# Performance work log

Hardware: AMD Instinct MI355X
Metric: run time of the kernel (lower is better)

The kernel has to match this reference:

```python
import jax, jax.numpy as jnp
import numpy as np

HIDDEN = 1024
N_EXPERTS = 8
CAP_FACTOR = 1.1
LN_EPS = 1e-5


def setup_inputs() -> dict:
    key = jax.random.key(0)
    ks = jax.random.split(key, 8)
    d, E, dff = HIDDEN, N_EXPERTS, 4 * HIDDEN
    x = jax.random.normal(ks[0], (4, 2048, d), dtype=jnp.float32)
    gate_w = jax.random.normal(ks[1], (d, E), dtype=jnp.float32) / np.sqrt(d)
    ln_g = jnp.ones((E, d), dtype=jnp.float32)
    ln_b = jnp.zeros((E, d), dtype=jnp.float32)
    w1 = jax.random.normal(ks[2], (E, d, dff), dtype=jnp.float32) / np.sqrt(d)
    b1 = jnp.zeros((E, dff), dtype=jnp.float32)
    w2 = jax.random.normal(ks[3], (E, dff, d), dtype=jnp.float32) / np.sqrt(dff)
    b2 = jnp.zeros((E, d), dtype=jnp.float32)
    return {"x": x, "gate_w": gate_w, "ln_g": ln_g, "ln_b": ln_b,
            "w1": w1, "b1": b1, "w2": w2, "b2": b2}


def reference(x, gate_w, ln_g, ln_b, w1, b1, w2, b2):
    B, S, d = x.shape
    E = gate_w.shape[1]
    N = B * S
    cap = int(N / E * CAP_FACTOR)  # expert capacity

    xt = x.reshape(N, d)
    # Router: top-1 expert per token (max-subtract before softmax is a no-op)
    logits = xt @ gate_w                               # [N, E]
    probs = jax.nn.softmax(logits, axis=-1)
    eidx = jnp.argmax(probs, axis=-1)                  # [N] int

    onehot = jax.nn.one_hot(eidx, E, dtype=jnp.int32)  # [N, E]
    counts = onehot.sum(axis=0).astype(jnp.float32)    # pre-drop counts [E]

    # Deterministic capacity: keep first `cap` tokens per expert, drop rest.
    # (torch code drops randomly via multinomial; structure is identical.)
    pos = jnp.cumsum(onehot, axis=0) - 1               # [N, E]
    pos_tok = jnp.take_along_axis(pos, eidx[:, None], axis=1)[:, 0]  # [N]
    keep = (pos_tok < cap).astype(x.dtype)             # [N]
    pos_c = jnp.minimum(pos_tok, cap - 1)              # clamp; dropped tokens write zeros

    # Dispatch into per-expert buffers [E, cap, d]
    buf = jnp.zeros((E, cap, d), dtype=x.dtype).at[eidx, pos_c].add(xt * keep[:, None])

    # Per-expert FFN: LayerNorm -> Linear -> GELU -> Linear
    mu = buf.mean(axis=-1, keepdims=True)
    var = jnp.mean((buf - mu) ** 2, axis=-1, keepdims=True)
    nb = (buf - mu) * jax.lax.rsqrt(var + LN_EPS)
    nb = nb * ln_g[:, None, :] + ln_b[:, None, :]
    h = jax.nn.gelu(jnp.einsum('ecd,edf->ecf', nb, w1) + b1[:, None, :], approximate=False)
    y = jnp.einsum('ecf,efd->ecd', h, w2) + b2[:, None, :]  # [E, cap, d]

    # Combine: dropped tokens get zeros (matches torch output init)
    out_tok = y[eidx, pos_c] * keep[:, None]           # [N, d]
    output = out_tok.reshape(B, S, d)

    # Load-balancing loss: 1 - cosine(counts, uniform) * 0.01
    tokens_per_expert = N / E
    uniform = jnp.full((E,), tokens_per_expert, dtype=jnp.float32)
    cos = jnp.dot(counts, uniform) / (jnp.linalg.norm(counts) * jnp.linalg.norm(uniform) + 1e-8)
    loss = 1.0 - cos * 0.01
    return output, loss
```

## Files before the change

kernel.cpp:

```cpp
#include <hip/hip_runtime.h>
#include <cstdint>
#include <cstddef>

#define NTOK 8192
#define D    1024
#define DFF  4096
#define NEXP 8
#define CAP  1126
#define MPAD 1152

typedef float f32x4 __attribute__((ext_vector_type(4)));
typedef __bf16 bf16x8 __attribute__((ext_vector_type(8)));

__device__ inline unsigned short f2bf(float f) {
    unsigned u = __float_as_uint(f);
    u += 0x7fffu + ((u >> 16) & 1u);
    return (unsigned short)(u >> 16);
}

__device__ inline float gelu(float x) {
    float z  = 0.70710678118654752f * x;
    float az = fabsf(z);
    float t  = 1.0f / fmaf(0.3275911f, az, 1.0f);
    float p  = t * fmaf(t, fmaf(t, fmaf(t, fmaf(t, 1.061405429f, -1.453152027f),
                                        1.421413741f), -0.284496736f), 0.254829592f);
    float ee = __expf(-az * az);
    float er = fmaf(-p, ee, 1.0f);
    er = __builtin_copysignf(er, z);
    return 0.5f * x * (1.0f + er);
}

__device__ inline void gload16(const void* g, void* l) {
    __builtin_amdgcn_global_load_lds(
        (const __attribute__((address_space(1))) unsigned int*)g,
        (__attribute__((address_space(3))) unsigned int*)l,
        16, 0, 0);
}

__global__ __launch_bounds__(256) void transpose_kernel(
    const float* __restrict__ W, unsigned short* __restrict__ WT, int K, int N)
{
    __shared__ __align__(16) char smem[32768];
    int tb = blockIdx.x;
    int tiles_k = K >> 7, tiles_n = N >> 7;
    int per_e = tiles_k * tiles_n;
    int e = tb / per_e, rem = tb % per_e;
    int kb = rem % tiles_k, nb = rem / tiles_k;
    const float* We = W + (size_t)e * K * N + (size_t)(kb * 128) * N + nb * 128;
    unsigned short* Oe = WT + (size_t)e * K * N + (size_t)(nb * 128) * K + kb * 128;
    float* lds = (float*)smem;
    int t = threadIdx.x;
    #pragma unroll
    for (int p = 0; p < 2; ++p) {
        __syncthreads();
        #pragma unroll
        for (int j = 0; j < 8; ++j) {
            int idx = j * 256 + t;
            int r = idx >> 5, c4 = idx & 31;
            const float4 v = *(const float4*)(We + (size_t)(p * 64 + r) * N + c4 * 4);
            *(float4*)(lds + r * 128 + c4 * 4) = v;
        }
        __syncthreads();
        int c = t >> 1, half = t & 1;
        const float* col = lds + (half * 32) * 128 + c;
        unsigned short* orow = Oe + (size_t)c * K + p * 64 + half * 32;
        #pragma unroll
        for (int q = 0; q < 4; ++q) {
            uint4 o;
            o.x = f2bf(col[(q*8+0)*128]) | ((unsigned)f2bf(col[(q*8+1)*128]) << 16);
            o.y = f2bf(col[(q*8+2)*128]) | ((unsigned)f2bf(col[(q*8+3)*128]) << 16);
            o.z = f2bf(col[(q*8+4)*128]) | ((unsigned)f2bf(col[(q*8+5)*128]) << 16);
            o.w = f2bf(col[(q*8+6)*128]) | ((unsigned)f2bf(col[(q*8+7)*128]) << 16);
            *(uint4*)(orow + q * 8) = o;
        }
    }
}

__global__ __launch_bounds__(256) void router_kernel(
    const float* __restrict__ x, const float* __restrict__ gw, int* __restrict__ eidx)
{
    int tok  = blockIdx.x * 4 + (threadIdx.x >> 6);
    int lane = threadIdx.x & 63;
    const float* xr = x + (size_t)tok * D;
    float a[8] = {0.f,0.f,0.f,0.f,0.f,0.f,0.f,0.f};
    #pragma unroll
    for (int it = 0; it < D / 64; ++it) {
        int d = lane + it * 64;
        float xv = xr[d];
        const float4 g0 = *(const float4*)(gw + (size_t)d * 8);
        const float4 g1 = *(const float4*)(gw + (size_t)d * 8 + 4);
        a[0] += xv * g0.x; a[1] += xv * g0.y; a[2] += xv * g0.z; a[3] += xv * g0.w;
        a[4] += xv * g1.x; a[5] += xv * g1.y; a[6] += xv * g1.z; a[7] += xv * g1.w;
    }
    #pragma unroll
    for (int off = 32; off > 0; off >>= 1)
        #pragma unroll
        for (int e = 0; e < 8; ++e) a[e] += __shfl_xor(a[e], off, 64);
    if (lane == 0) {
        int bi = 0; float bv = a[0];
        #pragma unroll
        for (int e = 1; e < 8; ++e) if (a[e] > bv) { bv = a[e]; bi = e; }
        eidx[tok] = bi;
    }
}

__global__ __launch_bounds__(1024) void scan_kernel(
    const int* __restrict__ eidx, int* __restrict__ slot_map,
    int* __restrict__ kept_cnt, float* __restrict__ loss_out,
    int* __restrict__ droplist, int* __restrict__ dropcnt)
{
    __shared__ int sc[8][1024];
    __shared__ int dcnt;
    int t = threadIdx.x;
    if (t == 0) dcnt = 0;
    int le[8];
    int c[8] = {0,0,0,0,0,0,0,0};
    #pragma unroll
    for (int i = 0; i < 8; ++i) { le[i] = eidx[t * 8 + i]; c[le[i]]++; }
    int v[8];
    #pragma unroll
    for (int e = 0; e < 8; ++e) { v[e] = c[e]; sc[e][t] = v[e]; }
    __syncthreads();
    for (int s = 1; s < 1024; s <<= 1) {
        int add[8] = {0,0,0,0,0,0,0,0};
        if (t >= s) {
            #pragma unroll
            for (int e = 0; e < 8; ++e) add[e] = sc[e][t - s];
        }
        __syncthreads();
        #pragma unroll
        for (int e = 0; e < 8; ++e) { v[e] += add[e]; sc[e][t] = v[e]; }
        __syncthreads();
    }
    int base[8];
    #pragma unroll
    for (int e = 0; e < 8; ++e) base[e] = v[e] - c[e];
    #pragma unroll
    for (int i = 0; i < 8; ++i) {
        int e = le[i]; int pos = base[e]++;
        if (pos < CAP) slot_map[e * CAP + pos] = t * 8 + i;
        else { int s = atomicAdd(&dcnt, 1); droplist[s] = t * 8 + i; }
    }
    __syncthreads();
    if (t == 0) *dropcnt = dcnt;
    if (t == 1023) {
        float dotv = 0.f, ss = 0.f;
        #pragma unroll
        for (int e = 0; e < 8; ++e) {
            float cf = (float)v[e];
            kept_cnt[e] = v[e] < CAP ? v[e] : CAP;
            dotv += cf * 1024.0f;
            ss   += cf * cf;
        }
        float denom = sqrtf(ss) * (1024.0f * sqrtf(8.0f)) + 1e-8f;
        loss_out[0] = 1.0f - 0.01f * (dotv / denom);
    }
}

__global__ __launch_bounds__(256) void zero_dropped(
    const int* __restrict__ droplist, const int* __restrict__ dropcnt,
    float4* __restrict__ out)
{
    int n = (*dropcnt) * 256;
    for (int idx = blockIdx.x * 256 + threadIdx.x; idx < n; idx += gridDim.x * 256)
        out[(size_t)droplist[idx >> 8] * 256 + (idx & 255)] = make_float4(0.f,0.f,0.f,0.f);
}

__global__ __launch_bounds__(256) void dispatch_ln(
    const float* __restrict__ x, const float* __restrict__ lng, const float* __restrict__ lnb,
    const int* __restrict__ slot_map, const int* __restrict__ kept_cnt,
    unsigned short* __restrict__ xbuf)
{
    int p = blockIdx.x, e = blockIdx.y, tid = threadIdx.x;
    ushort4* dst = (ushort4*)(xbuf + ((size_t)e * MPAD + p) * D) + tid;
    if (p >= kept_cnt[e]) { *dst = make_ushort4(0, 0, 0, 0); return; }
    int tok = slot_map[e * CAP + p];
    const float4 xv = *((const float4*)(x + (size_t)tok * D) + tid);
    float s  = xv.x + xv.y + xv.z + xv.w;
    float ss = xv.x * xv.x + xv.y * xv.y + xv.z * xv.z + xv.w * xv.w;
    #pragma unroll
    for (int off = 32; off > 0; off >>= 1) {
        s  += __shfl_xor(s,  off, 64);
        ss += __shfl_xor(ss, off, 64);
    }
    __shared__ float red[8];
    int lane = tid & 63, wv = tid >> 6;
    if (lane == 0) { red[wv] = s; red[4 + wv] = ss; }
    __syncthreads();
    s  = red[0] + red[1] + red[2] + red[3];
    ss = red[4] + red[5] + red[6] + red[7];
    float mu = s * (1.0f / D);
    float rs = rsqrtf(ss * (1.0f / D) - mu * mu + 1e-5f);
    const float4 gv = *((const float4*)(lng + (size_t)e * D) + tid);
    const float4 bv = *((const float4*)(lnb + (size_t)e * D) + tid);
    ushort4 o;
    o.x = f2bf((xv.x - mu) * rs * gv.x + bv.x);
    o.y = f2bf((xv.y - mu) * rs * gv.y + bv.y);
    o.z = f2bf((xv.z - mu) * rs * gv.z + bv.z);
    o.w = f2bf((xv.w - mu) * rs * gv.w + bv.w);
    *dst = o;
}

template<int K, int N, int MODE>
__global__ __launch_bounds__(256, 3) void gemm_kernel(
    const unsigned short* __restrict__ A,
    const unsigned short* __restrict__ BT,
    const float* __restrict__ bias,
    unsigned short* __restrict__ Hout,
    float* __restrict__ Yout,
    const int* __restrict__ slot_map,
    const int* __restrict__ kept_cnt)
{
    constexpr int MB = MPAD / 128;
    constexpr int NB = N / 128;
    constexpr int GB = NEXP * MB * NB;
    constexpr int T  = K / 32;
    __shared__ __align__(16) char smem[49152];

    const int obid = blockIdx.x;
    const int q8 = GB >> 3, r8 = GB & 7;
    const int xcd = obid & 7, ii = obid >> 3;
    const int swz = (xcd < r8 ? xcd * (q8 + 1) : r8 * (q8 + 1) + (xcd - r8) * q8) + ii;
    const int mb = swz % MB;
    const int t2 = swz / MB;
    const int nb = t2 % NB;
    const int e  = t2 / NB;

    const int tid  = threadIdx.x;
    const int lane = tid & 63;
    const int l15  = lane & 15, lg = lane >> 4;
    const int wave = tid >> 6, wr = wave >> 1, wc = wave & 1;
    const unsigned short* Ae = A + ((size_t)e * MPAD + (size_t)mb * 128) * K;
    const unsigned short* Be = BT + ((size_t)e * N + (size_t)nb * 128) * K;
    f32x4 acc[4][4] = {};

    auto stage = [&](int buf, int kk) {
        char* sA = smem + buf * 16384;
        char* sB = sA + 8192;
        #pragma unroll
        for (int q = 0; q < 2; ++q) {
            int cid = q * 256 + tid;
            int row = cid >> 2, pp = cid & 3;
            int cc  = pp ^ ((row >> 1) & 3);
            gload16(Ae + (size_t)row * K + kk * 32 + cc * 8, sA + cid * 16);
            gload16(Be + (size_t)row * K + kk * 32 + cc * 8, sB + cid * 16);
        }
    };
    auto compute = [&](int buf) {
        const char* sA = smem + buf * 16384;
        const char* sB = sA + 8192;
        bf16x8 af[4], bfr[4];
        #pragma unroll
        for (int i = 0; i < 4; ++i) {
            int ra = wr * 64 + i * 16 + l15;
            af[i]  = *(const bf16x8*)(sA + ra * 64 + ((lg ^ ((ra >> 1) & 3)) << 4));
            int rb = wc * 64 + i * 16 + l15;
            bfr[i] = *(const bf16x8*)(sB + rb * 64 + ((lg ^ ((rb >> 1) & 3)) << 4));
        }
        __builtin_amdgcn_s_setprio(1);
        #pragma unroll
        for (int mi = 0; mi < 4; ++mi)
            #pragma unroll
            for (int ni = 0; ni < 4; ++ni)
                acc[mi][ni] = __builtin_amdgcn_mfma_f32_16x16x32_bf16(
                    bfr[ni], af[mi], acc[mi][ni], 0, 0, 0);
        __builtin_amdgcn_s_setprio(0);
    };

    stage(0, 0);
    stage(1, 1);
    asm volatile("s_waitcnt vmcnt(4)" ::: "memory");
    __builtin_amdgcn_s_barrier();
    asm volatile("" ::: "memory");
    int b = 0;
    for (int t = 0; t < T - 2; ++t) {
        int bn = b + 2; if (bn >= 3) bn -= 3;
        stage(bn, t + 2);
        compute(b);
        asm volatile("s_waitcnt vmcnt(4) lgkmcnt(0)" ::: "memory");
        __builtin_amdgcn_s_barrier();
        asm volatile("" ::: "memory");
        b = (b == 2) ? 0 : b + 1;
    }
    compute(b);
    asm volatile("s_waitcnt vmcnt(0) lgkmcnt(0)" ::: "memory");
    __builtin_amdgcn_s_barrier();
    asm volatile("" ::: "memory");
    b = (b == 2) ? 0 : b + 1;
    compute(b);

    const int kept = (MODE == 1) ? kept_cnt[e] : 0;
    #pragma unroll
    for (int mi = 0; mi < 4; ++mi) {
        const int row = mb * 128 + wr * 64 + mi * 16 + l15;
        int tok = 0; bool live = true;
        if (MODE == 1) {
            live = row < kept;
            tok = live ? slot_map[e * CAP + row] : 0;
        }
        #pragma unroll
        for (int ni = 0; ni < 4; ++ni) {
            const int colb = nb * 128 + wc * 64 + ni * 16 + 4 * lg;
            const float4 bv = *(const float4*)(bias + (size_t)e * N + colb);
            if (MODE == 0) {
                ushort4 o;
                o.x = f2bf(gelu(acc[mi][ni][0] + bv.x));
                o.y = f2bf(gelu(acc[mi][ni][1] + bv.y));
                o.z = f2bf(gelu(acc[mi][ni][2] + bv.z));
                o.w = f2bf(gelu(acc[mi][ni][3] + bv.w));
                *(ushort4*)(Hout + ((size_t)e * MPAD + row) * N + colb) = o;
            } else if (live) {
                float4 o = make_float4(acc[mi][ni][0] + bv.x, acc[mi][ni][1] + bv.y,
                                       acc[mi][ni][2] + bv.z, acc[mi][ni][3] + bv.w);
                *(float4*)(Yout + (size_t)tok * D + colb) = o;
            }
        }
    }
}

extern "C" void kernel_launch(void* const* d_in, const int* in_sizes, int n_in,
                              void* d_out, int out_size, void* d_ws, size_t ws_size,
                              hipStream_t stream)
{
    const float* x   = (const float*)d_in[0];
    const float* gw  = (const float*)d_in[1];
    const float* lng = (const float*)d_in[2];
    const float* lnb = (const float*)d_in[3];
    const float* w1  = (const float*)d_in[4];
    const float* b1  = (const float*)d_in[5];
    const float* w2  = (const float*)d_in[6];
    const float* b2  = (const float*)d_in[7];
    float* out = (float*)d_out;
    char* ws = (char*)d_ws;

    unsigned short* wT   = (unsigned short*)ws;
    unsigned short* xbuf = (unsigned short*)(ws + 67108864);
    unsigned short* hbuf = (unsigned short*)(ws + 67108864 + 18874368);
    int* eidx     = (int*)(ws + 161480704);
    int* slot_map = eidx + NTOK;
    int* kept     = slot_map + NEXP * CAP;
    int* dropcnt  = kept + NEXP;
    int* droplist = dropcnt + 8;

    constexpr int GB1 = NEXP * (MPAD / 128) * (DFF / 128);
    constexpr int GB2 = NEXP * (MPAD / 128) * (D / 128);
    constexpr int TB  = 2048;

    router_kernel<<<NTOK / 4, 256, 0, stream>>>(x, gw, eidx);
    scan_kernel<<<1, 1024, 0, stream>>>(eidx, slot_map, kept,
                                        out + (size_t)NTOK * D, droplist, dropcnt);
    zero_dropped<<<64, 256, 0, stream>>>(droplist, dropcnt, (float4*)out);
    dispatch_ln<<<dim3(MPAD, NEXP), 256, 0, stream>>>(x, lng, lnb, slot_map, kept, xbuf);

    transpose_kernel<<<TB, 256, 0, stream>>>(w1, wT, D, DFF);
    gemm_kernel<D, DFF, 0><<<GB1, 256, 0, stream>>>(
        xbuf, wT, b1, hbuf, nullptr, slot_map, kept);

    transpose_kernel<<<TB, 256, 0, stream>>>(w2, wT, DFF, D);
    gemm_kernel<DFF, D, 1><<<GB2, 256, 0, stream>>>(
        hbuf, wT, b2, nullptr, out, slot_map, kept);
}
```

Baseline: 342.4 us.

## Fuse weight transposes into scan and dispatch kernels to overlap independent work

The w1 transpose now runs as extra blocks of the scan kernel, and the w2 transpose plus zeroing of dropped rows runs as extra blocks of the dispatch/LayerNorm kernel. Each weight matrix gets its own transposed buffer, and the buffers are rearranged so eidx and droplist sit inside hbuf. The scan is rewritten for 256 threads handling 32 tokens each. The goal is to cut kernel-launch count and let the serial single-block scan overlap with bandwidth-heavy transposes. The cost is a larger workspace, and the single scan block now has a longer serial loop.

```diff
diff --git a/kernel.cpp b/kernel.cpp
--- a/kernel.cpp
+++ b/kernel.cpp
@@ -37,11 +37,9 @@
         16, 0, 0);
 }
 
-__global__ __launch_bounds__(256) void transpose_kernel(
-    const float* __restrict__ W, unsigned short* __restrict__ WT, int K, int N)
-{
-    __shared__ __align__(16) char smem[32768];
-    int tb = blockIdx.x;
+__device__ void transpose_tile_dev(const float* __restrict__ W, unsigned short* __restrict__ WT,
+                                   int K, int N, int tb, char* smem)
+{
     int tiles_k = K >> 7, tiles_n = N >> 7;
     int per_e = tiles_k * tiles_n;
     int e = tb / per_e, rem = tb % per_e;
@@ -104,24 +102,30 @@
     }
 }
 
-__global__ __launch_bounds__(1024) void scan_kernel(
+__global__ __launch_bounds__(256) void fused_scan_trA(
     const int* __restrict__ eidx, int* __restrict__ slot_map,
     int* __restrict__ kept_cnt, float* __restrict__ loss_out,
-    int* __restrict__ droplist, int* __restrict__ dropcnt)
-{
-    __shared__ int sc[8][1024];
+    int* __restrict__ droplist, int* __restrict__ dropcnt,
+    const float* __restrict__ W1, unsigned short* __restrict__ WT1)
+{
+    __shared__ __align__(16) char smem[32768];
+    if (blockIdx.x > 0) {
+        transpose_tile_dev(W1, WT1, D, DFF, blockIdx.x - 1, smem);
+        return;
+    }
+    int (*sc)[256] = (int(*)[256])smem;
     __shared__ int dcnt;
     int t = threadIdx.x;
     if (t == 0) dcnt = 0;
-    int le[8];
+    int le[32];
     int c[8] = {0,0,0,0,0,0,0,0};
     #pragma unroll
-    for (int i = 0; i < 8; ++i) { le[i] = eidx[t * 8 + i]; c[le[i]]++; }
+    for (int i = 0; i < 32; ++i) { le[i] = eidx[t * 32 + i]; c[le[i]]++; }
     int v[8];
     #pragma unroll
     for (int e = 0; e < 8; ++e) { v[e] = c[e]; sc[e][t] = v[e]; }
     __syncthreads();
-    for (int s = 1; s < 1024; s <<= 1) {
+    for (int s = 1; s < 256; s <<= 1) {
         int add[8] = {0,0,0,0,0,0,0,0};
         if (t >= s) {
             #pragma unroll
@@ -136,14 +140,14 @@
     #pragma unroll
     for (int e = 0; e < 8; ++e) base[e] = v[e] - c[e];
     #pragma unroll
-    for (int i = 0; i < 8; ++i) {
+    for (int i = 0; i < 32; ++i) {
         int e = le[i]; int pos = base[e]++;
-        if (pos < CAP) slot_map[e * CAP + pos] = t * 8 + i;
-        else { int s = atomicAdd(&dcnt, 1); droplist[s] = t * 8 + i; }
+        if (pos < CAP) slot_map[e * CAP + pos] = t * 32 + i;
+        else { int s = atomicAdd(&dcnt, 1); droplist[s] = t * 32 + i; }
     }
     __syncthreads();
     if (t == 0) *dropcnt = dcnt;
-    if (t == 1023) {
+    if (t == 255) {
         float dotv = 0.f, ss = 0.f;
         #pragma unroll
         for (int e = 0; e < 8; ++e) {
@@ -157,21 +161,30 @@
     }
 }
 
-__global__ __launch_bounds__(256) void zero_dropped(
-    const int* __restrict__ droplist, const int* __restrict__ dropcnt,
-    float4* __restrict__ out)
-{
-    int n = (*dropcnt) * 256;
-    for (int idx = blockIdx.x * 256 + threadIdx.x; idx < n; idx += gridDim.x * 256)
-        out[(size_t)droplist[idx >> 8] * 256 + (idx & 255)] = make_float4(0.f,0.f,0.f,0.f);
-}
-
-__global__ __launch_bounds__(256) void dispatch_ln(
+#define TRB 2048
+#define ZB  64
+__global__ __launch_bounds__(256) void fused_disp_trB(
     const float* __restrict__ x, const float* __restrict__ lng, const float* __restrict__ lnb,
     const int* __restrict__ slot_map, const int* __restrict__ kept_cnt,
-    unsigned short* __restrict__ xbuf)
-{
-    int p = blockIdx.x, e = blockIdx.y, tid = threadIdx.x;
+    unsigned short* __restrict__ xbuf,
+    const int* __restrict__ droplist, const int* __restrict__ dropcnt,
+    float4* __restrict__ out,
+    const float* __restrict__ W2, unsigned short* __restrict__ WT2)
+{
+    __shared__ __align__(16) char smem[32768];
+    const int bid = blockIdx.x;
+    if (bid < TRB) {
+        transpose_tile_dev(W2, WT2, DFF, D, bid, smem);
+        return;
+    }
+    if (bid < TRB + ZB) {
+        int n = (*dropcnt) * 256;
+        for (int idx = (bid - TRB) * 256 + threadIdx.x; idx < n; idx += ZB * 256)
+            out[(size_t)droplist[idx >> 8] * 256 + (idx & 255)] = make_float4(0.f,0.f,0.f,0.f);
+        return;
+    }
+    int rem = bid - TRB - ZB;
+    int p = rem % MPAD, e = rem / MPAD, tid = threadIdx.x;
     ushort4* dst = (ushort4*)(xbuf + ((size_t)e * MPAD + p) * D) + tid;
     if (p >= kept_cnt[e]) { *dst = make_ushort4(0, 0, 0, 0); return; }
     int tok = slot_map[e * CAP + p];
@@ -183,7 +196,7 @@
         s  += __shfl_xor(s,  off, 64);
         ss += __shfl_xor(ss, off, 64);
     }
-    __shared__ float red[8];
+    float* red = (float*)smem;
     int lane = tid & 63, wv = tid >> 6;
     if (lane == 0) { red[wv] = s; red[4 + wv] = ss; }
     __syncthreads();
@@ -333,30 +346,26 @@
     float* out = (float*)d_out;
     char* ws = (char*)d_ws;
 
-    unsigned short* wT   = (unsigned short*)ws;
-    unsigned short* xbuf = (unsigned short*)(ws + 67108864);
-    unsigned short* hbuf = (unsigned short*)(ws + 67108864 + 18874368);
-    int* eidx     = (int*)(ws + 161480704);
-    int* slot_map = eidx + NTOK;
+    unsigned short* wT1  = (unsigned short*)ws;
+    unsigned short* wT2  = (unsigned short*)(ws + 67108864);
+    unsigned short* xbuf = (unsigned short*)(ws + 134217728);
+    unsigned short* hbuf = (unsigned short*)(ws + 153092096);
+    int* slot_map = (int*)(ws + 228589568);
     int* kept     = slot_map + NEXP * CAP;
     int* dropcnt  = kept + NEXP;
-    int* droplist = dropcnt + 8;
+    int* eidx     = (int*)hbuf;
+    int* droplist = (int*)hbuf + NTOK;
 
     constexpr int GB1 = NEXP * (MPAD / 128) * (DFF / 128);
     constexpr int GB2 = NEXP * (MPAD / 128) * (D / 128);
-    constexpr int TB  = 2048;
 
     router_kernel<<<NTOK / 4, 256, 0, stream>>>(x, gw, eidx);
-    scan_kernel<<<1, 1024, 0, stream>>>(eidx, slot_map, kept,
-                                        out + (size_t)NTOK * D, droplist, dropcnt);
-    zero_dropped<<<64, 256, 0, stream>>>(droplist, dropcnt, (float4*)out);
-    dispatch_ln<<<dim3(MPAD, NEXP), 256, 0, stream>>>(x, lng, lnb, slot_map, kept, xbuf);
-
-    transpose_kernel<<<TB, 256, 0, stream>>>(w1, wT, D, DFF);
+    fused_scan_trA<<<1 + 2048, 256, 0, stream>>>(
+        eidx, slot_map, kept, out + (size_t)NTOK * D, droplist, dropcnt, w1, wT1);
+    fused_disp_trB<<<TRB + ZB + MPAD * NEXP, 256, 0, stream>>>(
+        x, lng, lnb, slot_map, kept, xbuf, droplist, dropcnt, (float4*)out, w2, wT2);
     gemm_kernel<D, DFF, 0><<<GB1, 256, 0, stream>>>(
-        xbuf, wT, b1, hbuf, nullptr, slot_map, kept);
-
-    transpose_kernel<<<TB, 256, 0, stream>>>(w2, wT, DFF, D);
+        xbuf, wT1, b1, hbuf, nullptr, slot_map, kept);
     gemm_kernel<DFF, D, 1><<<GB2, 256, 0, stream>>>(
-        hbuf, wT, b2, nullptr, out, slot_map, kept);
-}
+        hbuf, wT2, b2, nullptr, out, slot_map, kept);
+}
```

Result: no change. 341.3 us (-0.3%).
